# Kernel optimization log

Hardware: AMD Instinct MI355X
Metric: run time of the kernel (lower is better)

The kernel has to match this reference:

```python
import jax, jax.numpy as jnp
import numpy as np
import math

D_MODEL = 1024
NUM_HEADS = 16
D_FF = 4096
EPS = 1e-5
BATCH = 2
SEQ = 2048


def _trunc_normal(key, shape, std):
    # truncated normal on [-3std, 3std], matching nn.init.trunc_normal_
    return std * jax.random.truncated_normal(key, -3.0, 3.0, shape, dtype=jnp.float32)


def setup_inputs() -> dict:
    key = jax.random.key(0)
    ks = jax.random.split(key, 8)
    x = jax.random.normal(ks[0], (BATCH, SEQ, D_MODEL), dtype=jnp.float32)
    std_dd = math.sqrt(2.0 / (D_MODEL + D_MODEL))
    std_up = math.sqrt(2.0 / (D_MODEL + D_FF))
    # Linear stores W as [out_features, in_features]; forward does x @ W.T
    W_q = _trunc_normal(ks[1], (D_MODEL, D_MODEL), std_dd)
    W_k = _trunc_normal(ks[2], (D_MODEL, D_MODEL), std_dd)
    W_v = _trunc_normal(ks[3], (D_MODEL, D_MODEL), std_dd)
    W_o = _trunc_normal(ks[4], (D_MODEL, D_MODEL), std_dd)
    W1 = _trunc_normal(ks[5], (D_FF, D_MODEL), std_up)
    W2 = _trunc_normal(ks[6], (D_MODEL, D_FF), std_up)
    ln1_w = jnp.ones((D_MODEL,), jnp.float32)
    ln1_b = jnp.zeros((D_MODEL,), jnp.float32)
    ln2_w = jnp.ones((D_MODEL,), jnp.float32)
    ln2_b = jnp.zeros((D_MODEL,), jnp.float32)
    return {"x": x, "W_q": W_q, "W_k": W_k, "W_v": W_v, "W_o": W_o,
            "W1": W1, "W2": W2,
            "ln1_w": ln1_w, "ln1_b": ln1_b, "ln2_w": ln2_w, "ln2_b": ln2_b}


def _layernorm(x, w, b):
    xf = x.astype(jnp.float32)
    mean = xf.mean(axis=-1, keepdims=True)
    var = jnp.mean((xf - mean) ** 2, axis=-1, keepdims=True)
    xn = (xf - mean) / jnp.sqrt(var + EPS)
    return (xn * w.astype(jnp.float32) + b.astype(jnp.float32)).astype(x.dtype)


def _attention(x, W_q, W_k, W_v, W_o):
    B, S, D = x.shape
    H, dk = NUM_HEADS, D // NUM_HEADS
    Q = (x @ W_q.T).reshape(B, S, H, dk).transpose(0, 2, 1, 3)  # [B,H,S,dk]
    K = (x @ W_k.T).reshape(B, S, H, dk).transpose(0, 2, 1, 3)
    V = (x @ W_v.T).reshape(B, S, H, dk).transpose(0, 2, 1, 3)
    scores = jnp.einsum('bhqd,bhkd->bhqk', Q, K) / math.sqrt(dk)
    causal = jnp.tril(jnp.ones((S, S), dtype=bool))
    scores = jnp.where(causal, scores, -jnp.inf)
    attn = jax.nn.softmax(scores, axis=-1)
    out = jnp.einsum('bhqk,bhkd->bhqd', attn, V)  # [B,H,S,dk]
    out = out.transpose(0, 2, 1, 3).reshape(B, S, D)
    return out @ W_o.T


def _ffn(x, W1, W2):
    h = x @ W1.T
    h = h * (h > 0)  # ReLU
    return h @ W2.T


def reference(x, W_q, W_k, W_v, W_o, W1, W2, ln1_w, ln1_b, ln2_w, ln2_b):
    x = x + _attention(_layernorm(x, ln1_w, ln1_b), W_q, W_k, W_v, W_o)
    x = x + _ffn(_layernorm(x, ln2_w, ln2_b), W1, W2)
    return x
```

## Files before the change

kernel.cpp:

```cpp
#include <hip/hip_runtime.h>
#include <stdint.h>

typedef unsigned short u16;
typedef unsigned int u32;
typedef __bf16 bf16x8 __attribute__((ext_vector_type(8)));
typedef float f32x4 __attribute__((ext_vector_type(4)));
typedef unsigned short u16x8 __attribute__((ext_vector_type(8)));
typedef unsigned short u16x4 __attribute__((ext_vector_type(4)));
typedef u16x8 u16x8_a __attribute__((may_alias));
typedef u16x4 u16x4_a __attribute__((may_alias));

#define DEV static __device__ __forceinline__

DEV u16 f2bf(float f) {
  unsigned u = __builtin_bit_cast(unsigned, f);
  u += 0x7fffu + ((u >> 16) & 1u);
  return (u16)(u >> 16);
}
DEV bf16x8 ld8(const u16* p) {
  u16x8 v = *(const u16x8_a*)p;
  return __builtin_bit_cast(bf16x8, v);
}
DEV f32x4 vmax4(f32x4 a, f32x4 b) {
  f32x4 r;
  r[0] = fmaxf(a[0], b[0]); r[1] = fmaxf(a[1], b[1]);
  r[2] = fmaxf(a[2], b[2]); r[3] = fmaxf(a[3], b[3]);
  return r;
}
DEV void swz_block(int& bx, int& by) {
  const int gx = gridDim.x;
  const int nwg = gx * gridDim.y;
  int lin = by * gx + bx;
  const int q = nwg >> 3, r = nwg & 7, x = lin & 7, p = lin >> 3;
  lin = (x < r ? x * (q + 1) : r * (q + 1) + (x - r) * q) + p;
  bx = lin % gx; by = lin / gx;
}

#define GL_LDS16(gp, lp)                                                        \
  __builtin_amdgcn_global_load_lds(                                             \
      (const __attribute__((address_space(1))) void*)(gp),                      \
      (__attribute__((address_space(3))) void*)(lp), 16, 0, 0)

#define VMW4 asm volatile("s_waitcnt vmcnt(4)" ::: "memory")
#define VMW2 asm volatile("s_waitcnt vmcnt(2)" ::: "memory")
#define VMW0 asm volatile("s_waitcnt vmcnt(0)" ::: "memory")
#define BAR  __builtin_amdgcn_s_barrier()

struct Cvt6 {
  const float* s[6];
  u16* d[6];
  int n4[6];
};
__global__ __launch_bounds__(256) void cvt6_k(Cvt6 c) {
  const int yi = blockIdx.y;
  const int i = blockIdx.x * 256 + threadIdx.x;
  if (i < c.n4[yi]) {
    float4 v = ((const float4*)c.s[yi])[i];
    u16x4 o;
    o[0] = f2bf(v.x); o[1] = f2bf(v.y); o[2] = f2bf(v.z); o[3] = f2bf(v.w);
    *(u16x4_a*)(c.d[yi] + (size_t)i * 4) = o;
  }
}

__global__ __launch_bounds__(256) void red_k(const float* __restrict__ p,
                                             float* __restrict__ d, int n4) {
  int i = blockIdx.x * 256 + threadIdx.x;
  if (i < n4) {
    float4 a = ((const float4*)d)[i];
    float4 b = ((const float4*)p)[i];
    a.x += b.x; a.y += b.y; a.z += b.z; a.w += b.w;
    ((float4*)d)[i] = a;
  }
}

__global__ __launch_bounds__(256) void ln_k(const float* __restrict__ x,
                                            const float* __restrict__ w,
                                            const float* __restrict__ b,
                                            u16* __restrict__ o) {
  const int row = blockIdx.x, t = threadIdx.x;
  const float4 v = ((const float4*)(x + (size_t)row * 1024))[t];
  float s = v.x + v.y + v.z + v.w;
  float q = v.x * v.x + v.y * v.y + v.z * v.z + v.w * v.w;
#pragma unroll
  for (int m = 1; m < 64; m <<= 1) { s += __shfl_xor(s, m); q += __shfl_xor(q, m); }
  __shared__ float ss[4], qq[4];
  if ((t & 63) == 0) { ss[t >> 6] = s; qq[t >> 6] = q; }
  __syncthreads();
  s = ss[0] + ss[1] + ss[2] + ss[3];
  q = qq[0] + qq[1] + qq[2] + qq[3];
  const float mean = s * (1.f / 1024.f);
  const float var = q * (1.f / 1024.f) - mean * mean;
  const float rstd = rsqrtf(var + 1e-5f);
  const float4 wv = ((const float4*)w)[t];
  const float4 bv = ((const float4*)b)[t];
  u16x4 ov;
  ov[0] = f2bf((v.x - mean) * rstd * wv.x + bv.x);
  ov[1] = f2bf((v.y - mean) * rstd * wv.y + bv.y);
  ov[2] = f2bf((v.z - mean) * rstd * wv.z + bv.z);
  ov[3] = f2bf((v.w - mean) * rstd * wv.w + bv.w);
  *(u16x4_a*)(o + (size_t)row * 1024 + t * 4) = ov;
}

__global__ __launch_bounds__(256) void vtr_k(const u16* __restrict__ qkvV,
                                             u16* __restrict__ vt) {
  __shared__ u16 T[64][65];
  const int st = blockIdx.x, bh = blockIdx.y;
  const int b = bh >> 4, h = bh & 15;
  const int t = threadIdx.x;
  const u16* src = qkvV + ((size_t)(b * 2048 + st * 64)) * 3072 + h * 64;
  const int r = t >> 2, c0 = (t & 3) * 16;
  u16x8 a0 = *(const u16x8_a*)(src + (size_t)r * 3072 + c0);
  u16x8 a1 = *(const u16x8_a*)(src + (size_t)r * 3072 + c0 + 8);
#pragma unroll
  for (int e = 0; e < 8; ++e) { T[r][c0 + e] = a0[e]; T[r][c0 + 8 + e] = a1[e]; }
  __syncthreads();
  const int d = t >> 2, s0 = (t & 3) * 16;
  u16x8 o0, o1;
#pragma unroll
  for (int e = 0; e < 8; ++e) { o0[e] = T[s0 + e][d]; o1[e] = T[s0 + 8 + e][d]; }
  u16* dst = vt + ((size_t)bh * 64 + d) * 2048 + (size_t)st * 64 + s0;
  *(u16x8_a*)dst = o0;
  *(u16x8_a*)(dst + 8) = o1;
}

DEV void stage_op(const u16* __restrict__ G, int K, int kk, u16* lds, int set,
                  int isB, int w, int l) {
#pragma unroll
  for (int i = 0; i < 2; ++i) {
    const int c = i * 8 + w;
    int rb;
    if (!isB) { const int lr = c * 8; rb = (lr < 64 ? lr : lr + 64) + set * 64; }
    else      { rb = (c >> 2) * 64 + set * 32 + (c & 3) * 8; }
    const int row = rb + (l >> 3);
    const int c8 = (l & 7) ^ (row & 7);
    GL_LDS16(G + (size_t)row * K + kk + c8 * 8, lds + rb * 64);
  }
}
DEV void rdA(const u16* as, int wr, int mh, int l15, int l4, bf16x8 af[4][2]) {
#pragma unroll
  for (int f = 0; f < 4; ++f) {
    const int row = wr * 128 + mh * 64 + f * 16 + l15;
#pragma unroll
    for (int ks = 0; ks < 2; ++ks) {
      const int c8 = (ks * 4 + l4) ^ (row & 7);
      af[f][ks] = ld8(as + row * 64 + c8 * 8);
    }
  }
}
DEV void rdB(const u16* bs, int wc, int nh, int l15, int l4, bf16x8 bf_[2][2]) {
#pragma unroll
  for (int g = 0; g < 2; ++g) {
    const int row = wc * 64 + nh * 32 + g * 16 + l15;
#pragma unroll
    for (int ks = 0; ks < 2; ++ks) {
      const int c8 = (ks * 4 + l4) ^ (row & 7);
      bf_[g][ks] = ld8(bs + row * 64 + c8 * 8);
    }
  }
}

#define MFMA16(mh, nh)                                                          \
  __builtin_amdgcn_s_setprio(1);                                                \
  _Pragma("unroll")                                                             \
  for (int f = 0; f < 4; ++f) {                                                 \
    _Pragma("unroll")                                                           \
    for (int g = 0; g < 2; ++g) {                                               \
      f32x4& a_ = acc[(mh) * 4 + f][(nh) * 2 + g];                              \
      a_ = __builtin_amdgcn_mfma_f32_16x16x32_bf16(af[f][0], bfr[g][0], a_, 0, 0, 0); \
      a_ = __builtin_amdgcn_mfma_f32_16x16x32_bf16(af[f][1], bfr[g][1], a_, 0, 0, 0); \
    }                                                                           \
  }                                                                             \
  __builtin_amdgcn_s_setprio(0);

template <int EPI>
__global__ __launch_bounds__(512, 2) void gemm8(const u16* __restrict__ A,
                                                const u16* __restrict__ Bw,
                                                u16* __restrict__ Cp,
                                                int M, int N, int K, int qcols) {
  __shared__ __align__(16) u16 As[2][256 * 64];
  __shared__ __align__(16) u16 Bs[2][256 * 64];
  const int t = threadIdx.x, w = t >> 6, l = t & 63;
  const int l15 = l & 15, l4 = l >> 4;
  const int wr = w >> 2, wc = w & 3;
  int bx = blockIdx.x, by = blockIdx.y;
  swz_block(bx, by);
  const int bm0 = by * 256, bn0 = bx * 256;
  const u16* Ab = A + (size_t)bm0 * K;
  const u16* Bb = Bw + (size_t)bn0 * K;

  f32x4 acc[8][4] = {};
  stage_op(Ab, K, 0, As[0], 0, 0, w, l);
  stage_op(Bb, K, 0, Bs[0], 0, 1, w, l);
  stage_op(Bb, K, 0, Bs[0], 1, 1, w, l);
  stage_op(Ab, K, 0, As[0], 1, 0, w, l);
  VMW4;
  BAR;

  const int nk = K >> 6;
  int cur = 0;
  bf16x8 af[4][2], bfr[2][2];
  for (int kt = 0; kt < nk; ++kt) {
    const int kn = (kt + 1) << 6;
    const bool more = (kt + 1 < nk);
    u16* An = As[cur ^ 1];
    u16* Bn = Bs[cur ^ 1];
    rdA(As[cur], wr, 0, l15, l4, af);
    rdB(Bs[cur], wc, 0, l15, l4, bfr);
    if (more) stage_op(Ab, K, kn, An, 0, 0, w, l);
    BAR;
    MFMA16(0, 0)
    if (more) { VMW4; } else { VMW2; }
    BAR;
    rdB(Bs[cur], wc, 1, l15, l4, bfr);
    if (more) stage_op(Bb, K, kn, Bn, 0, 1, w, l);
    BAR;
    MFMA16(0, 1)
    if (more) { VMW4; } else { VMW0; }
    BAR;
    rdA(As[cur], wr, 1, l15, l4, af);
    if (more) stage_op(Bb, K, kn, Bn, 1, 1, w, l);
    BAR;
    MFMA16(1, 1)
    BAR;
    rdB(Bs[cur], wc, 0, l15, l4, bfr);
    if (more) stage_op(Ab, K, kn, An, 1, 0, w, l);
    BAR;
    MFMA16(1, 0)
    if (more) { VMW4; }
    BAR;
    cur ^= 1;
  }

#pragma unroll
  for (int m = 0; m < 8; ++m) {
    const int row0 = bm0 + wr * 128 + m * 16 + l4 * 4;
#pragma unroll
    for (int n = 0; n < 4; ++n) {
      const int col = bn0 + wc * 64 + n * 16 + l15;
      const float qs = (col < qcols) ? 0.18033688f : 1.f;
#pragma unroll
      for (int r = 0; r < 4; ++r) {
        float v = acc[m][n][r] * qs;
        if constexpr (EPI == 1) v = v > 0.f ? v : 0.f;
        Cp[(size_t)(row0 + r) * N + col] = f2bf(v);
      }
    }
  }
}

__global__ __launch_bounds__(256, 2) void gemm64(const u16* __restrict__ A,
                                                 const u16* __restrict__ Bw,
                                                 float* __restrict__ C,
                                                 const float* __restrict__ res,
                                                 int M, int N, int K) {
  __shared__ __align__(16) u16 As[2][64 * 64];
  __shared__ __align__(16) u16 Bs[2][128 * 64];
  const int t = threadIdx.x, w = t >> 6, l = t & 63;
  const int l15 = l & 15, l4 = l >> 4;
  const int wr = w >> 1, wc = w & 1;
  int bx = blockIdx.x, by = blockIdx.y;
  swz_block(bx, by);
  const int bm0 = by * 64, bn0 = bx * 128;
  const u16* Ab = A + (size_t)bm0 * K;
  const u16* Bb = Bw + (size_t)bn0 * K;

  auto stgA = [&](int buf, int kk) {
#pragma unroll
    for (int i = 0; i < 2; ++i) {
      const int s = t + i * 256;
      const int row = s >> 3;
      const int c8 = (l & 7) ^ (row & 7);
      GL_LDS16(Ab + (size_t)row * K + kk + c8 * 8, &As[buf][(s >> 6) * 512]);
    }
  };
  auto stgB = [&](int buf, int kk) {
#pragma unroll
    for (int i = 0; i < 4; ++i) {
      const int s = t + i * 256;
      const int row = s >> 3;
      const int c8 = (l & 7) ^ (row & 7);
      GL_LDS16(Bb + (size_t)row * K + kk + c8 * 8, &Bs[buf][(s >> 6) * 512]);
    }
  };

  f32x4 acc[2][4] = {};
  stgA(0, 0); stgB(0, 0);
  const int nk = K >> 6;
  int cur = 0;
  for (int kt = 0; kt < nk; ++kt) {
    __syncthreads();
    if (kt + 1 < nk) { stgA(cur ^ 1, (kt + 1) << 6); stgB(cur ^ 1, (kt + 1) << 6); }
    bf16x8 af[2][2], bfr[4][2];
#pragma unroll
    for (int f = 0; f < 2; ++f) {
      const int row = wr * 32 + f * 16 + l15;
#pragma unroll
      for (int ks = 0; ks < 2; ++ks)
        af[f][ks] = ld8(&As[cur][row * 64 + (((ks * 4 + l4) ^ (row & 7)) * 8)]);
    }
#pragma unroll
    for (int n = 0; n < 4; ++n) {
      const int row = wc * 64 + n * 16 + l15;
#pragma unroll
      for (int ks = 0; ks < 2; ++ks)
        bfr[n][ks] = ld8(&Bs[cur][row * 64 + (((ks * 4 + l4) ^ (row & 7)) * 8)]);
    }
    __builtin_amdgcn_s_setprio(1);
#pragma unroll
    for (int f = 0; f < 2; ++f)
#pragma unroll
      for (int n = 0; n < 4; ++n) {
        acc[f][n] = __builtin_amdgcn_mfma_f32_16x16x32_bf16(af[f][0], bfr[n][0], acc[f][n], 0, 0, 0);
        acc[f][n] = __builtin_amdgcn_mfma_f32_16x16x32_bf16(af[f][1], bfr[n][1], acc[f][n], 0, 0, 0);
      }
    __builtin_amdgcn_s_setprio(0);
    __syncthreads();
    cur ^= 1;
  }

#pragma unroll
  for (int f = 0; f < 2; ++f) {
    const int row0 = bm0 + wr * 32 + f * 16 + l4 * 4;
#pragma unroll
    for (int n = 0; n < 4; ++n) {
      const int col = bn0 + wc * 64 + n * 16 + l15;
#pragma unroll
      for (int r = 0; r < 4; ++r) {
        const size_t idx = (size_t)(row0 + r) * N + col;
        C[idx] = res[idx] + acc[f][n][r];
      }
    }
  }
}

__global__ __launch_bounds__(256, 2) void gemm128s(const u16* __restrict__ A,
                                                   const u16* __restrict__ Bw,
                                                   float* __restrict__ C,
                                                   float* __restrict__ P,
                                                   const float* __restrict__ res,
                                                   int M, int N, int K, int Kc) {
  __shared__ __align__(16) u16 As[2][128 * 64];
  __shared__ __align__(16) u16 Bs[2][128 * 64];
  const int t = threadIdx.x, w = t >> 6, l = t & 63;
  const int l15 = l & 15, l4 = l >> 4;
  const int wr = w >> 1, wc = w & 1;
  int bx = blockIdx.x, by = blockIdx.y;
  swz_block(bx, by);
  const int kz = blockIdx.z;
  const int bm0 = by * 128, bn0 = bx * 128;
  const u16* Ab = A + (size_t)bm0 * K + (size_t)kz * Kc;
  const u16* Bb = Bw + (size_t)bn0 * K + (size_t)kz * Kc;

  auto stg = [&](const u16* __restrict__ G, u16* lds, int kk) {
#pragma unroll
    for (int i = 0; i < 4; ++i) {
      const int s = t + i * 256;
      const int row = s >> 3;
      const int c8 = (l & 7) ^ (row & 7);
      GL_LDS16(G + (size_t)row * K + kk + c8 * 8, lds + (s >> 6) * 512);
    }
  };

  f32x4 acc[4][4] = {};
  stg(Ab, As[0], 0); stg(Bb, Bs[0], 0);
  const int nk = Kc >> 6;
  int cur = 0;
  for (int kt = 0; kt < nk; ++kt) {
    __syncthreads();
    if (kt + 1 < nk) {
      stg(Ab, As[cur ^ 1], (kt + 1) << 6);
      stg(Bb, Bs[cur ^ 1], (kt + 1) << 6);
    }
    bf16x8 af[4][2], bfr[4][2];
#pragma unroll
    for (int f = 0; f < 4; ++f) {
      const int row = wr * 64 + f * 16 + l15;
#pragma unroll
      for (int ks = 0; ks < 2; ++ks)
        af[f][ks] = ld8(&As[cur][row * 64 + (((ks * 4 + l4) ^ (row & 7)) * 8)]);
    }
#pragma unroll
    for (int n = 0; n < 4; ++n) {
      const int row = wc * 64 + n * 16 + l15;
#pragma unroll
      for (int ks = 0; ks < 2; ++ks)
        bfr[n][ks] = ld8(&Bs[cur][row * 64 + (((ks * 4 + l4) ^ (row & 7)) * 8)]);
    }
    __builtin_amdgcn_s_setprio(1);
#pragma unroll
    for (int f = 0; f < 4; ++f)
#pragma unroll
      for (int n = 0; n < 4; ++n) {
        acc[f][n] = __builtin_amdgcn_mfma_f32_16x16x32_bf16(af[f][0], bfr[n][0], acc[f][n], 0, 0, 0);
        acc[f][n] = __builtin_amdgcn_mfma_f32_16x16x32_bf16(af[f][1], bfr[n][1], acc[f][n], 0, 0, 0);
      }
    __builtin_amdgcn_s_setprio(0);
    __syncthreads();
    cur ^= 1;
  }

#pragma unroll
  for (int f = 0; f < 4; ++f) {
    const int row0 = bm0 + wr * 64 + f * 16 + l4 * 4;
#pragma unroll
    for (int n = 0; n < 4; ++n) {
      const int col = bn0 + wc * 64 + n * 16 + l15;
#pragma unroll
      for (int r = 0; r < 4; ++r) {
        const size_t idx = (size_t)(row0 + r) * N + col;
        if (kz == 0) C[idx] = res[idx] + acc[f][n][r];
        else         P[idx] = acc[f][n][r];
      }
    }
  }
}

__global__ __launch_bounds__(256) void attn_k(const u16* __restrict__ Qm,
                                              const u16* __restrict__ Km,
                                              const u16* __restrict__ vt,
                                              u16* __restrict__ Om) {
  const int S = 2048, D = 1024, ldq = 3072;
  int p = blockIdx.x, bh = blockIdx.y;
  swz_block(p, bh);
  const int bb = bh >> 4, h = bh & 15;
  const int t = threadIdx.x, w = t >> 6, l = t & 63, l15 = l & 15, l4 = l >> 4;
  const float NEGINF = -__builtin_inff();

  __shared__ __align__(16) u16 Ksm[2][64 * 64];
  __shared__ __align__(16) u16 Vsm[2][64 * 64];
  __shared__ __align__(16) u32 Psm[4][16 * 32];

  const u16* Qb = Qm + (size_t)bb * S * ldq + h * 64;
  const u16* Kb = Km + (size_t)bb * S * ldq + h * 64;
  const u16* Vtb = vt + (size_t)bh * 64 * 2048;

  auto stageKV = [&](int j, int buf) {
    const int k0 = j * 64;
#pragma unroll
    for (int i = 0; i < 2; ++i) {
      const int s = t + i * 256;
      const int row = s >> 3;
      const int colE = ((s & 7) ^ (row & 7)) * 8;
      GL_LDS16(Kb + (size_t)(k0 + row) * ldq + colE, &Ksm[buf][(s >> 6) * 512]);
      GL_LDS16(Vtb + (size_t)row * 2048 + k0 + colE, &Vsm[buf][(s >> 6) * 512]);
    }
  };

  u32* Pw = &Psm[w][0];
  const u16* Pu = (const u16*)Pw;
  const int h7 = l15 & 7;

  for (int half = 0; half < 2; ++half) {
    const int bx = half ? (31 - p) : p;
    const int q0 = bx * 64;
    __syncthreads();
    stageKV(0, 0);

    bf16x8 qf[2];
    const int qq = q0 + w * 16 + l15;
#pragma unroll
    for (int c = 0; c < 2; ++c) qf[c] = ld8(Qb + (size_t)qq * ldq + c * 32 + l4 * 8);

    f32x4 accT[4] = {};
    float mrow = NEGINF, lrow = 0.f;
    int cur = 0;

    for (int j = 0; j <= bx; ++j) {
      __syncthreads();
      if (j < bx) stageKV(j + 1, cur ^ 1);

      f32x4 sv[4] = {};
      __builtin_amdgcn_s_setprio(1);
#pragma unroll
      for (int c = 0; c < 2; ++c) {
#pragma unroll
        for (int nf = 0; nf < 4; ++nf) {
          const int row = nf * 16 + l15;
          bf16x8 kf = ld8(&Ksm[cur][row * 64 + ((c * 32 + l4 * 8) ^ ((row & 7) * 8))]);
          sv[nf] = __builtin_amdgcn_mfma_f32_16x16x32_bf16(kf, qf[c], sv[nf], 0, 0, 0);
        }
      }
      __builtin_amdgcn_s_setprio(0);

      if (j == bx) {
        const int k0 = j * 64;
#pragma unroll
        for (int nf = 0; nf < 4; ++nf) {
          const int kb = k0 + nf * 16 + l4 * 4;
#pragma unroll
          for (int r = 0; r < 4; ++r)
            if (kb + r > qq) sv[nf][r] = NEGINF;
        }
      }

      f32x4 m4 = vmax4(vmax4(sv[0], sv[1]), vmax4(sv[2], sv[3]));
      float mt = fmaxf(fmaxf(m4[0], m4[1]), fmaxf(m4[2], m4[3]));
      mt = fmaxf(mt, __shfl_xor(mt, 16));
      mt = fmaxf(mt, __shfl_xor(mt, 32));
      const bool skip = __all(mt - mrow <= 11.54f);
      const float mnew = skip ? mrow : fmaxf(mrow, mt);
      if (!skip) {
        const float sf = __builtin_amdgcn_exp2f(mrow - mnew);
        lrow *= sf;
#pragma unroll
        for (int nf = 0; nf < 4; ++nf) accT[nf] *= sf;
        mrow = mnew;
      }
#pragma unroll
      for (int nf = 0; nf < 4; ++nf)
#pragma unroll
        for (int r = 0; r < 4; ++r)
          sv[nf][r] = __builtin_amdgcn_exp2f(sv[nf][r] - mnew);
      f32x4 s4 = (sv[0] + sv[1]) + (sv[2] + sv[3]);
      float ps = (s4[0] + s4[1]) + (s4[2] + s4[3]);
      ps += __shfl_xor(ps, 16);
      ps += __shfl_xor(ps, 32);
      lrow += ps;

#pragma unroll
      for (int nf = 0; nf < 4; ++nf) {
        u32 lo, hi;
        asm("v_cvt_pk_bf16_f32 %0, %1, %2" : "=v"(lo) : "v"(sv[nf][0]), "v"(sv[nf][1]));
        asm("v_cvt_pk_bf16_f32 %0, %1, %2" : "=v"(hi) : "v"(sv[nf][2]), "v"(sv[nf][3]));
        const int kw4 = (nf * 2 + (l4 >> 1)) ^ h7;
        const int base = l15 * 32 + kw4 * 4 + (l4 & 1) * 2;
        Pw[base] = lo;
        Pw[base + 1] = hi;
      }

      __builtin_amdgcn_s_setprio(1);
#pragma unroll
      for (int c = 0; c < 2; ++c) {
        bf16x8 pf = ld8(Pu + l15 * 64 + ((c * 4 + l4) ^ h7) * 8);
#pragma unroll
        for (int nf = 0; nf < 4; ++nf) {
          const int row = nf * 16 + l15;
          bf16x8 vf = ld8(&Vsm[cur][row * 64 + ((c * 32 + l4 * 8) ^ ((row & 7) * 8))]);
          accT[nf] = __builtin_amdgcn_mfma_f32_16x16x32_bf16(vf, pf, accT[nf], 0, 0, 0);
        }
      }
      __builtin_amdgcn_s_setprio(0);
      cur ^= 1;
    }

    const float inv = 1.f / lrow;
    u16* orow = Om + ((size_t)bb * S + qq) * D + h * 64;
#pragma unroll
    for (int nf = 0; nf < 4; ++nf) {
      u16x4 ov;
#pragma unroll
      for (int r = 0; r < 4; ++r) ov[r] = f2bf(accT[nf][r] * inv);
      *(u16x4_a*)(orow + nf * 16 + l4 * 4) = ov;
    }
  }
}

extern "C" void kernel_launch(void* const* d_in, const int* in_sizes, int n_in,
                              void* d_out, int out_size, void* d_ws, size_t ws_size,
                              hipStream_t stream) {
  (void)in_sizes; (void)n_in; (void)out_size; (void)ws_size;
  const float* x    = (const float*)d_in[0];
  const float* W_q  = (const float*)d_in[1];
  const float* W_k  = (const float*)d_in[2];
  const float* W_v  = (const float*)d_in[3];
  const float* W_o  = (const float*)d_in[4];
  const float* W1   = (const float*)d_in[5];
  const float* W2   = (const float*)d_in[6];
  const float* ln1w = (const float*)d_in[7];
  const float* ln1b = (const float*)d_in[8];
  const float* ln2w = (const float*)d_in[9];
  const float* ln2b = (const float*)d_in[10];

  const size_t MB = 1ull << 20;
  char* W = (char*)d_ws;
  u16* wqkv  = (u16*)(W + 0);
  u16* wo    = (u16*)(W + 6 * MB);
  u16* w1b   = (u16*)(W + 8 * MB);
  u16* w2b   = (u16*)(W + 16 * MB);
  u16* xn1   = (u16*)(W + 24 * MB);
  u16* qkv   = (u16*)(W + 32 * MB);
  u16* attnb = (u16*)(W + 56 * MB);
  u16* vt    = (u16*)(W + 64 * MB);
  u16* xn2   = (u16*)(W + 64 * MB);
  u16* hbuf  = (u16*)(W + 24 * MB);
  float* fpart = (float*)(W + 56 * MB);
  float* x2  = (float*)d_out;

  Cvt6 c;
  c.s[0] = W_q; c.d[0] = wqkv;              c.n4[0] = 1 << 18;
  c.s[1] = W_k; c.d[1] = wqkv + (1 << 20);  c.n4[1] = 1 << 18;
  c.s[2] = W_v; c.d[2] = wqkv + (2 << 20);  c.n4[2] = 1 << 18;
  c.s[3] = W_o; c.d[3] = wo;                c.n4[3] = 1 << 18;
  c.s[4] = W1;  c.d[4] = w1b;               c.n4[4] = 1 << 20;
  c.s[5] = W2;  c.d[5] = w2b;               c.n4[5] = 1 << 20;
  cvt6_k<<<dim3(4096, 6), dim3(256), 0, stream>>>(c);

  ln_k<<<dim3(4096), dim3(256), 0, stream>>>(x, ln1w, ln1b, xn1);
  gemm8<0><<<dim3(12, 16), dim3(512), 0, stream>>>(xn1, wqkv, qkv, 4096, 3072, 1024, 1024);
  vtr_k<<<dim3(32, 32), dim3(256), 0, stream>>>(qkv + 2048, vt);
  attn_k<<<dim3(16, 32), dim3(256), 0, stream>>>(qkv, qkv + 1024, vt, attnb);
  gemm64<<<dim3(8, 64), dim3(256), 0, stream>>>(attnb, wo, x2, x, 4096, 1024, 1024);
  ln_k<<<dim3(4096), dim3(256), 0, stream>>>(x2, ln2w, ln2b, xn2);
  gemm8<1><<<dim3(16, 16), dim3(512), 0, stream>>>(xn2, w1b, hbuf, 4096, 4096, 1024, 0);
  gemm128s<<<dim3(8, 32, 2), dim3(256), 0, stream>>>(hbuf, w2b, x2, fpart, x2,
                                                     4096, 1024, 4096, 2048);
  red_k<<<dim3(4096), dim3(256), 0, stream>>>(fpart, x2, 1 << 20);
}
```

Before: 228.7 us.

## Replace FFN down-projection GEMM with 8-wave 128x256 ping-pong pipelined kernel

The W2 split-K GEMM moves from a 256-thread 128x128 tile kernel to a 512-thread 128x256 tile kernel (gemm8s), matching the gemm8 style used elsewhere. Each K-step is split into four quarter-phases that interleave LDS fragment reads, staged global-to-LDS loads of the next tile, and MFMA blocks, with fine-grained vmcnt waits and barriers. The goal is better overlap of memory traffic with matrix math and more reuse of A per tile. The cost is more barriers per K-step and a grid that halves to 256 blocks, which may leave CUs underused.

```diff
diff --git a/kernel.cpp b/kernel.cpp
--- a/kernel.cpp
+++ b/kernel.cpp
@@ -42,7 +42,9 @@
       (__attribute__((address_space(3))) void*)(lp), 16, 0, 0)
 
 #define VMW4 asm volatile("s_waitcnt vmcnt(4)" ::: "memory")
+#define VMW3 asm volatile("s_waitcnt vmcnt(3)" ::: "memory")
 #define VMW2 asm volatile("s_waitcnt vmcnt(2)" ::: "memory")
+#define VMW1 asm volatile("s_waitcnt vmcnt(1)" ::: "memory")
 #define VMW0 asm volatile("s_waitcnt vmcnt(0)" ::: "memory")
 #define BAR  __builtin_amdgcn_s_barrier()
 
@@ -333,83 +335,128 @@
   }
 }
 
-__global__ __launch_bounds__(256, 2) void gemm128s(const u16* __restrict__ A,
-                                                   const u16* __restrict__ Bw,
-                                                   float* __restrict__ C,
-                                                   float* __restrict__ P,
-                                                   const float* __restrict__ res,
-                                                   int M, int N, int K, int Kc) {
+DEV void s_stgA(const u16* __restrict__ G, int K, int kk, u16* lds, int set,
+                int w, int l) {
+  const int c = w;
+  const int rb = (c >> 2) * 64 + set * 32 + (c & 3) * 8;
+  const int row = rb + (l >> 3);
+  const int c8 = (l & 7) ^ (row & 7);
+  GL_LDS16(G + (size_t)row * K + kk + c8 * 8, lds + rb * 64);
+}
+DEV void s_stgB(const u16* __restrict__ G, int K, int kk, u16* lds, int set,
+                int w, int l) {
+#pragma unroll
+  for (int i = 0; i < 2; ++i) {
+    const int c = i * 8 + w;
+    const int rb = (c >> 2) * 64 + set * 32 + (c & 3) * 8;
+    const int row = rb + (l >> 3);
+    const int c8 = (l & 7) ^ (row & 7);
+    GL_LDS16(G + (size_t)row * K + kk + c8 * 8, lds + rb * 64);
+  }
+}
+DEV void s_rdA(const u16* as, int wr, int mh, int l15, int l4, bf16x8 af[2][2]) {
+#pragma unroll
+  for (int f = 0; f < 2; ++f) {
+    const int row = wr * 64 + mh * 32 + f * 16 + l15;
+#pragma unroll
+    for (int ks = 0; ks < 2; ++ks)
+      af[f][ks] = ld8(as + row * 64 + (((ks * 4 + l4) ^ (row & 7)) * 8));
+  }
+}
+DEV void s_rdB(const u16* bs, int wc, int nh, int l15, int l4, bf16x8 bf_[2][2]) {
+#pragma unroll
+  for (int g = 0; g < 2; ++g) {
+    const int row = wc * 64 + nh * 32 + g * 16 + l15;
+#pragma unroll
+    for (int ks = 0; ks < 2; ++ks)
+      bf_[g][ks] = ld8(bs + row * 64 + (((ks * 4 + l4) ^ (row & 7)) * 8));
+  }
+}
+#define MFMA8(mh, nh)                                                           \
+  __builtin_amdgcn_s_setprio(1);                                                \
+  _Pragma("unroll")                                                             \
+  for (int f = 0; f < 2; ++f) {                                                 \
+    _Pragma("unroll")                                                           \
+    for (int g = 0; g < 2; ++g) {                                               \
+      f32x4& a_ = acc[(mh) * 2 + f][(nh) * 2 + g];                              \
+      a_ = __builtin_amdgcn_mfma_f32_16x16x32_bf16(af[f][0], bfr[g][0], a_, 0, 0, 0); \
+      a_ = __builtin_amdgcn_mfma_f32_16x16x32_bf16(af[f][1], bfr[g][1], a_, 0, 0, 0); \
+    }                                                                           \
+  }                                                                             \
+  __builtin_amdgcn_s_setprio(0);
+
+__global__ __launch_bounds__(512, 2) void gemm8s(const u16* __restrict__ A,
+                                                 const u16* __restrict__ Bw,
+                                                 float* __restrict__ C,
+                                                 float* __restrict__ P,
+                                                 const float* __restrict__ res,
+                                                 int M, int N, int K, int Kc) {
   __shared__ __align__(16) u16 As[2][128 * 64];
-  __shared__ __align__(16) u16 Bs[2][128 * 64];
+  __shared__ __align__(16) u16 Bs[2][256 * 64];
   const int t = threadIdx.x, w = t >> 6, l = t & 63;
   const int l15 = l & 15, l4 = l >> 4;
-  const int wr = w >> 1, wc = w & 1;
+  const int wr = w >> 2, wc = w & 3;
   int bx = blockIdx.x, by = blockIdx.y;
   swz_block(bx, by);
   const int kz = blockIdx.z;
-  const int bm0 = by * 128, bn0 = bx * 128;
+  const int bm0 = by * 128, bn0 = bx * 256;
   const u16* Ab = A + (size_t)bm0 * K + (size_t)kz * Kc;
   const u16* Bb = Bw + (size_t)bn0 * K + (size_t)kz * Kc;
 
-  auto stg = [&](const u16* __restrict__ G, u16* lds, int kk) {
-#pragma unroll
-    for (int i = 0; i < 4; ++i) {
-      const int s = t + i * 256;
-      const int row = s >> 3;
-      const int c8 = (l & 7) ^ (row & 7);
-      GL_LDS16(G + (size_t)row * K + kk + c8 * 8, lds + (s >> 6) * 512);
-    }
-  };
-
   f32x4 acc[4][4] = {};
-  stg(Ab, As[0], 0); stg(Bb, Bs[0], 0);
+  s_stgA(Ab, K, 0, As[0], 0, w, l);
+  s_stgB(Bb, K, 0, Bs[0], 0, w, l);
+  s_stgB(Bb, K, 0, Bs[0], 1, w, l);
+  s_stgA(Ab, K, 0, As[0], 1, w, l);
+  VMW3;
+  BAR;
+
   const int nk = Kc >> 6;
   int cur = 0;
+  bf16x8 af[2][2], bfr[2][2];
   for (int kt = 0; kt < nk; ++kt) {
-    __syncthreads();
-    if (kt + 1 < nk) {
-      stg(Ab, As[cur ^ 1], (kt + 1) << 6);
-      stg(Bb, Bs[cur ^ 1], (kt + 1) << 6);
-    }
-    bf16x8 af[4][2], bfr[4][2];
-#pragma unroll
-    for (int f = 0; f < 4; ++f) {
-      const int row = wr * 64 + f * 16 + l15;
-#pragma unroll
-      for (int ks = 0; ks < 2; ++ks)
-        af[f][ks] = ld8(&As[cur][row * 64 + (((ks * 4 + l4) ^ (row & 7)) * 8)]);
-    }
-#pragma unroll
-    for (int n = 0; n < 4; ++n) {
-      const int row = wc * 64 + n * 16 + l15;
-#pragma unroll
-      for (int ks = 0; ks < 2; ++ks)
-        bfr[n][ks] = ld8(&Bs[cur][row * 64 + (((ks * 4 + l4) ^ (row & 7)) * 8)]);
-    }
-    __builtin_amdgcn_s_setprio(1);
-#pragma unroll
-    for (int f = 0; f < 4; ++f)
-#pragma unroll
-      for (int n = 0; n < 4; ++n) {
-        acc[f][n] = __builtin_amdgcn_mfma_f32_16x16x32_bf16(af[f][0], bfr[n][0], acc[f][n], 0, 0, 0);
-        acc[f][n] = __builtin_amdgcn_mfma_f32_16x16x32_bf16(af[f][1], bfr[n][1], acc[f][n], 0, 0, 0);
-      }
-    __builtin_amdgcn_s_setprio(0);
-    __syncthreads();
+    const int kn = (kt + 1) << 6;
+    const bool more = (kt + 1 < nk);
+    u16* An = As[cur ^ 1];
+    u16* Bn = Bs[cur ^ 1];
+    s_rdA(As[cur], wr, 0, l15, l4, af);
+    s_rdB(Bs[cur], wc, 0, l15, l4, bfr);
+    if (more) s_stgA(Ab, K, kn, An, 0, w, l);
+    BAR;
+    MFMA8(0, 0)
+    if (more) { VMW2; } else { VMW1; }
+    BAR;
+    s_rdB(Bs[cur], wc, 1, l15, l4, bfr);
+    if (more) s_stgB(Bb, K, kn, Bn, 0, w, l);
+    BAR;
+    MFMA8(0, 1)
+    if (more) { VMW3; } else { VMW0; }
+    BAR;
+    s_rdA(As[cur], wr, 1, l15, l4, af);
+    if (more) s_stgB(Bb, K, kn, Bn, 1, w, l);
+    BAR;
+    MFMA8(1, 1)
+    BAR;
+    s_rdB(Bs[cur], wc, 0, l15, l4, bfr);
+    if (more) s_stgA(Ab, K, kn, An, 1, w, l);
+    BAR;
+    MFMA8(1, 0)
+    if (more) { VMW3; }
+    BAR;
     cur ^= 1;
   }
 
 #pragma unroll
-  for (int f = 0; f < 4; ++f) {
-    const int row0 = bm0 + wr * 64 + f * 16 + l4 * 4;
-#pragma unroll
-    for (int n = 0; n < 4; ++n) {
-      const int col = bn0 + wc * 64 + n * 16 + l15;
+  for (int fi = 0; fi < 4; ++fi) {
+    const int row0 = bm0 + wr * 64 + fi * 16 + l4 * 4;
+#pragma unroll
+    for (int gi = 0; gi < 4; ++gi) {
+      const int col = bn0 + wc * 64 + gi * 16 + l15;
 #pragma unroll
       for (int r = 0; r < 4; ++r) {
         const size_t idx = (size_t)(row0 + r) * N + col;
-        if (kz == 0) C[idx] = res[idx] + acc[f][n][r];
-        else         P[idx] = acc[f][n][r];
+        if (kz == 0) C[idx] = res[idx] + acc[fi][gi][r];
+        else         P[idx] = acc[fi][gi][r];
       }
     }
   }
@@ -602,7 +649,7 @@
   gemm64<<<dim3(8, 64), dim3(256), 0, stream>>>(attnb, wo, x2, x, 4096, 1024, 1024);
   ln_k<<<dim3(4096), dim3(256), 0, stream>>>(x2, ln2w, ln2b, xn2);
   gemm8<1><<<dim3(16, 16), dim3(512), 0, stream>>>(xn2, w1b, hbuf, 4096, 4096, 1024, 0);
-  gemm128s<<<dim3(8, 32, 2), dim3(256), 0, stream>>>(hbuf, w2b, x2, fpart, x2,
-                                                     4096, 1024, 4096, 2048);
+  gemm8s<<<dim3(4, 32, 2), dim3(512), 0, stream>>>(hbuf, w2b, x2, fpart, x2,
+                                                   4096, 1024, 4096, 2048);
   red_k<<<dim3(4096), dim3(256), 0, stream>>>(fpart, x2, 1 << 20);
 }
```

New measurement: 242.6 us. 6.1% more time.
